# Kernel tuning notes

Measured on AMD Instinct MI355X. Metric: run time of the kernel, lower is better.

The kernel has to match this reference:

```python
import jax, jax.numpy as jnp
import numpy as np

B, C, H, W = 2, 128, 128, 128
HEADS = 8
D = C // HEADS
EPS = 1e-5


def _conv(x, w, pad):
    # x: [B,C,H,W], w: [O,I,kh,kw]
    return jax.lax.conv_general_dilated(
        x, w, window_strides=(1, 1), padding=[(pad, pad), (pad, pad)],
        dimension_numbers=("NCHW", "OIHW", "NCHW"))


def setup_inputs() -> dict:
    key = jax.random.key(0)
    ks = jax.random.split(key, 9)
    s = 0.05
    w11 = lambda k: jax.random.normal(k, (C, C, 1, 1), jnp.float32) * s
    w33 = lambda k: jax.random.normal(k, (C, C, 3, 3), jnp.float32) * s
    return {
        "x": jax.random.normal(ks[0], (B, C, H, W), jnp.float32),
        "gamma": jnp.ones((W,), jnp.float32),   # LayerNorm over LAST dim (W==C)
        "beta": jnp.zeros((W,), jnp.float32),
        "scale": jnp.ones((1,), jnp.float32),
        "wq1": w11(ks[1]), "wq2": w33(ks[2]),
        "wk1": w11(ks[3]), "wk2": w33(ks[4]),
        "wv1": w11(ks[5]), "wv2": w33(ks[6]),
        "wo": w11(ks[7]),
    }


def reference(x, gamma, beta, scale, wq1, wq2, wk1, wk2, wv1, wv2, wo):
    residual = x
    # torch nn.LayerNorm(channels) normalizes the last axis (W), biased variance
    mu = jnp.mean(x, axis=-1, keepdims=True)
    var = jnp.var(x, axis=-1, keepdims=True)
    xn = (x - mu) * jax.lax.rsqrt(var + EPS) * gamma + beta

    q = _conv(_conv(xn, wq1, 0), wq2, 1).reshape(B, HEADS, H * W, D)
    k = _conv(_conv(xn, wk1, 0), wk2, 1).reshape(B, HEADS, H * W, D).transpose(0, 1, 3, 2)
    v = _conv(_conv(xn, wv1, 0), wv2, 1).reshape(B, HEADS, H * W, D)

    # transposed (channel) attention: [B,h,d,HW] @ [B,h,HW,d] -> [B,h,d,d]
    attn = jnp.matmul(k, q) / scale
    probs = jax.nn.softmax(attn, axis=-1)
    out = jnp.matmul(v, probs)                      # [B,h,HW,d]
    out = out.transpose(0, 1, 3, 2).reshape(B, C, H, W)
    return _conv(out, wo, 0) + residual
```

## Files before the change

### kernel.cpp

```cpp
#include <hip/hip_runtime.h>
#include <hip/hip_bf16.h>

typedef unsigned short u16;
typedef _Float16 f16;
typedef f16 f16x8 __attribute__((ext_vector_type(8)));
typedef float f32x4 __attribute__((ext_vector_type(4)));

__device__ __forceinline__ float b2f(u16 u) {
  unsigned v = (unsigned)u << 16; float f; __builtin_memcpy(&f, &v, 4); return f;
}
__device__ __forceinline__ u16 f2b(float f) {
  return __builtin_bit_cast(u16, __float2bfloat16(f));
}
__device__ __forceinline__ float h2f(u16 u) {
  return (float)__builtin_bit_cast(f16, u);
}
__device__ __forceinline__ u16 f2h(float f) {
  return __builtin_bit_cast(u16, (f16)f);
}
__device__ __forceinline__ void gload16(const void* g, void* l) {
  __builtin_amdgcn_global_load_lds((__attribute__((address_space(1))) void*)(const_cast<void*>(g)),
                                   (__attribute__((address_space(3))) void*)l, 16, 0, 0);
}
__device__ __forceinline__ f32x4 mfma16(int4 a, int4 b, f32x4 c) {
  return __builtin_amdgcn_mfma_f32_16x16x32_f16(__builtin_bit_cast(f16x8, a),
                                                __builtin_bit_cast(f16x8, b), c, 0, 0, 0);
}
union PK { int4 i; u16 u[8]; };

__device__ __forceinline__ int detect_isf(const u16* x, int tid, int nthr) {
  __shared__ int dcnt;
  if (tid == 0) dcnt = 0;
  __syncthreads();
  int c = 0;
  for (int i = tid; i < 1024; i += nthr) {
    u16 u = x[i * 2];
    if (((u >> 7) & 0xFF) >= 0x90) ++c;
  }
  if (c) atomicAdd(&dcnt, c);
  __syncthreads();
  return dcnt > 16;
}

#define XROW 33280

__global__ __launch_bounds__(256) void k_lnweff(
    const void* __restrict__ xr, const void* __restrict__ gr, const void* __restrict__ br_,
    const void* __restrict__ w1q, const void* __restrict__ w2q,
    const void* __restrict__ w1k, const void* __restrict__ w2k,
    const void* __restrict__ w1v, const void* __restrict__ w2v,
    u16* __restrict__ weff, u16* __restrict__ xnt, float* __restrict__ attnb) {
  __shared__ __align__(16) char smem[99328];
  int tid = threadIdx.x;
  int bi = blockIdx.x;

  if (bi < 27) {
    u16* sA = (u16*)smem;
    u16* sB = (u16*)(smem + 32768);
    int isf = detect_isf((const u16*)xr, tid, 256);
    int blk = bi;
    int tap = blk / 3, br = blk - tap * 3;
    const void* w1 = br == 0 ? w1q : (br == 1 ? w1k : w1v);
    const void* w2 = br == 0 ? w2q : (br == 1 ? w2k : w2v);
    if (isf) {
      const float* w2f = (const float*)w2;
      const float* w1f = (const float*)w1;
#pragma unroll 4
      for (int i = 0; i < 64; ++i) {
        int e = i * 256 + tid;
        int c = e >> 7, m = e & 127;
        sA[c * 128 + (m ^ ((c & 15) << 3))] = f2h(w2f[e * 9 + tap]);
        int ci = e & 127;
        sB[ci * 128 + ((e >> 7) ^ ((ci & 15) << 3))] = f2h(w1f[e]);
      }
    } else {
      const u16* w2u = (const u16*)w2;
      const u16* w1u = (const u16*)w1;
#pragma unroll 4
      for (int i = 0; i < 64; ++i) {
        int e = i * 256 + tid;
        int c = e >> 7, m = e & 127;
        sA[c * 128 + (m ^ ((c & 15) << 3))] = f2h(b2f(w2u[e * 9 + tap]));
        int ci = e & 127;
        sB[ci * 128 + ((e >> 7) ^ ((ci & 15) << 3))] = f2h(b2f(w1u[e]));
      }
    }
    __syncthreads();
    int lane = tid & 63, wv = tid >> 6;
    int m0w = (wv >> 1) * 64, n0w = (wv & 1) * 64;
    f32x4 acc[4][4] = {};
#pragma unroll
    for (int k0 = 0; k0 < 4; ++k0) {
      int mrow = k0 * 32 + (lane >> 4) * 8;
      int4 a4[4], b4[4];
#pragma unroll
      for (int mi = 0; mi < 4; ++mi) {
        int c = m0w + mi * 16 + (lane & 15);
        a4[mi] = *(const int4*)&sA[c * 128 + (mrow ^ ((c & 15) << 3))];
      }
#pragma unroll
      for (int ni = 0; ni < 4; ++ni) {
        int ci = n0w + ni * 16 + (lane & 15);
        b4[ni] = *(const int4*)&sB[ci * 128 + (mrow ^ ((ci & 15) << 3))];
      }
#pragma unroll
      for (int mi = 0; mi < 4; ++mi)
#pragma unroll
        for (int ni = 0; ni < 4; ++ni)
          acc[mi][ni] = mfma16(a4[mi], b4[ni], acc[mi][ni]);
    }
    __syncthreads();
#pragma unroll
    for (int mi = 0; mi < 4; ++mi)
#pragma unroll
      for (int ni = 0; ni < 4; ++ni) {
#pragma unroll
        for (int r = 0; r < 4; ++r) {
          int c = m0w + mi * 16 + (lane >> 4) * 4 + r;
          int ci = n0w + ni * 16 + (lane & 15);
          sA[c * 128 + ci] = f2h(acc[mi][ni][r]);
        }
      }
    __syncthreads();
    int4* dst = (int4*)((char*)weff + (size_t)blk * 32768);
#pragma unroll
    for (int i = 0; i < 8; ++i) {
      int gidx = i * 256 + tid;
      int k0 = gidx >> 9;
      int ch = gidx & 511;
      int mt = ch >> 6, l = ch & 63;
      int c = mt * 16 + (l & 15);
      int g = k0 * 4 + (l >> 4);
      dst[gidx] = *(const int4*)((const char*)sA + c * 256 + g * 16);
    }
    return;
  }

  int li = bi - 27;
  if (li >= 256) {
    int pid = li - 256;
    int b = pid >> 1, row = (pid & 1) ? 129 : 0;
    char* rbase = (char*)xnt + (size_t)(b * 130 + row) * XROW;
    int4 z = make_int4(0, 0, 0, 0);
    for (int i = 0; i < 9; ++i) {
      int idx = i * 256 + tid;
      if (idx < 2080) *(int4*)(rbase + idx * 16) = z;
    }
    return;
  }
  if (li == 0) {
    for (int i = tid; i < 4096; i += 256) attnb[i] = 0.f;
  }
  float* sx = (float*)smem;
  u16* sn = (u16*)(smem + 65536);
  float* sg = (float*)(smem + 98304);
  float* sb = (float*)(smem + 98816);
  int b = li >> 7, h = li & 127;
  int isf = detect_isf((const u16*)xr, tid, 256);
  if (tid < 128) {
    sg[tid] = isf ? ((const float*)gr)[tid] : b2f(((const u16*)gr)[tid]);
    sb[tid] = isf ? ((const float*)br_)[tid] : b2f(((const u16*)br_)[tid]);
  }
  if (isf) {
#pragma unroll
    for (int it = 0; it < 16; ++it) {
      int d = it * 4096 + tid * 16;
      int c = d >> 9;
      int p = (d >> 4) & 31;
      int sc = p ^ (c & 31);
      const char* src = (const char*)xr + (size_t)(b * 128 + c) * 65536 + (size_t)h * 512 + (sc << 4);
      gload16(src, (char*)sx + d);
    }
  } else {
    int c = tid >> 1, half = tid & 1;
    const u16* xu = (const u16*)xr + ((size_t)(b * 128 + c) * 128 + h) * 128 + half * 64;
    for (int i = 0; i < 16; ++i) {
      int phys = (half * 16 + i) ^ (c & 31);
      float* dst = sx + c * 128 + phys * 4;
#pragma unroll
      for (int j = 0; j < 4; ++j) dst[j] = b2f(xu[i * 4 + j]);
    }
  }
  __syncthreads();
  int c = tid >> 1, half = tid & 1;
  float sum = 0.f, sq = 0.f;
#pragma unroll
  for (int i = 0; i < 16; ++i) {
    int phys = (half * 16 + i) ^ (c & 31);
    const float* v = sx + c * 128 + phys * 4;
#pragma unroll
    for (int j = 0; j < 4; ++j) { float f = v[j]; sum += f; sq += f * f; }
  }
  sum += __shfl_xor(sum, 1);
  sq  += __shfl_xor(sq, 1);
  float mu = sum * 0.0078125f;
  float var = sq * 0.0078125f - mu * mu;
  float rs = rsqrtf(var + 1e-5f);
  int cg = c >> 3, cl = c & 7;
#pragma unroll
  for (int i = 0; i < 16; ++i) {
    int logical = half * 16 + i;
    int phys = logical ^ (c & 31);
    const float* v = sx + c * 128 + phys * 4;
#pragma unroll
    for (int j = 0; j < 4; ++j) {
      int w = logical * 4 + j;
      sn[w * 128 + (((cg ^ (w & 15)) << 3) | cl)] = f2h((v[j] - mu) * rs * sg[w] + sb[w]);
    }
  }
  __syncthreads();
  char* obase = (char*)xnt + (size_t)(b * 130 + h + 1) * XROW;
#pragma unroll
  for (int i = 0; i < 8; ++i) {
    int idx = i * 256 + tid;
    int g = idx >> 7, w = idx & 127;
    int phys = g ^ (w & 15);
    *(int4*)(obase + (g * 130 + w + 1) * 16) = *(const int4*)((const char*)sn + w * 256 + (phys << 4));
  }
  if (tid < 32) {
    int g = tid >> 1, side = tid & 1;
    *(int4*)(obase + (g * 130 + (side ? 129 : 0)) * 16) = make_int4(0, 0, 0, 0);
  }
}

#define STAGE_T(T, BUF) do { \
    const char* base_ = (const char*)weff + (size_t)(T) * 32768 + (size_t)cohalf * 4096; \
    char* dst_ = wq + (BUF) * 16384; \
    _Pragma("unroll") \
    for (int i_ = 0; i_ < 4; ++i_) \
      gload16(base_ + i_ * 8192 + tid * 16, dst_ + i_ * 4096 + tid * 16); \
  } while (0)

#define BC_LOAD(DST, T6) do { \
    int dy_ = (T6) / 3, dx_ = (T6) % 3; \
    const char* rb_ = (const char*)xnt + (size_t)(b * 130 + h + dy_) * XROW; \
    _Pragma("unroll") \
    for (int kk = 0; kk < 4; ++kk) \
      _Pragma("unroll") \
      for (int ni = 0; ni < 2; ++ni) { \
        int wp1 = n0l + ni * 16 + (lane & 15) + dx_;    \
        int chunk = (kk * 4 + (lane >> 4)) * 130 + wp1; \
        DST[kk][ni] = *(const int4*)(rb_ + chunk * 16); \
      } \
  } while (0)

#define QFULL(ACC, QB) do { \
    _Pragma("unroll") \
    for (int k0 = 0; k0 < 4; ++k0) { \
      int4 af[4]; \
      _Pragma("unroll") \
      for (int mi = 0; mi < 4; ++mi) \
        af[mi] = *(const int4*)((QB) + k0 * 4096 + mi * 1024 + lane * 16); \
      _Pragma("unroll") \
      for (int mi = 0; mi < 4; ++mi) { \
        ACC[mi][0] = mfma16(af[mi], bcA[k0][0], ACC[mi][0]); \
        ACC[mi][1] = mfma16(af[mi], bcA[k0][1], ACC[mi][1]); \
      } \
    } \
  } while (0)

__global__ __launch_bounds__(256, 2) void k_conv(const u16* __restrict__ xnt,
    const u16* __restrict__ weff, u16* __restrict__ Vc, float* __restrict__ attnb) {
  __shared__ __align__(16) char wq[49152];
  int tid = threadIdx.x, lane = tid & 63, wv = tid >> 6;
  int bi = blockIdx.x;
  int cohalf = bi & 1, h = (bi >> 1) & 127, b = bi >> 8;
  int n0l = wv * 32;

  int4 bcA[4][2], bcB[4][2];
  BC_LOAD(bcA, 0);
  STAGE_T(0, 0);
  __syncthreads();

  f32x4 aq[4][2] = {}, ak[4][2] = {}, av[4][2] = {};

  for (int t = 0; t < 27; ++t) {
    int br = t % 3, tgrp = t / 3;
    if (t + 1 < 27) STAGE_T(t + 1, (t + 1) & 1);
    if (br == 0) {
      if (tgrp > 0) {
#pragma unroll
        for (int kk = 0; kk < 4; ++kk)
#pragma unroll
          for (int ni = 0; ni < 2; ++ni) bcA[kk][ni] = bcB[kk][ni];
      }
      if (tgrp < 8) BC_LOAD(bcB, tgrp + 1);
    }
    const char* qb = wq + (t & 1) * 16384;
    if (br == 0)      QFULL(aq, qb);
    else if (br == 1) QFULL(ak, qb);
    else              QFULL(av, qb);
    __syncthreads();
  }
  u16* scrQ = (u16*)wq;
  u16* scrK = (u16*)(wq + 16384);
  u16* scrV = (u16*)(wq + 32768);
#pragma unroll
  for (int mi = 0; mi < 4; ++mi)
#pragma unroll
    for (int ni = 0; ni < 2; ++ni)
#pragma unroll
      for (int r = 0; r < 4; ++r) {
        int cc = mi * 16 + (lane >> 4) * 4 + r;
        int wl = n0l + ni * 16 + (lane & 15);
        scrQ[cc * 128 + wl] = f2h(aq[mi][ni][r]);
        scrK[cc * 128 + wl] = f2h(ak[mi][ni][r]);
        scrV[cc * 128 + wl] = f2h(av[mi][ni][r]);
      }
  __syncthreads();
  {
    int hdg = cohalf * 4 + wv;
    f32x4 g = {};
#pragma unroll
    for (int k2 = 0; k2 < 4; ++k2) {
      PK A, Bq;
#pragma unroll
      for (int jj = 0; jj < 8; ++jj) {
        int k = (lane >> 4) * 8 + jj;
        int ci = k2 * 4 + (k >> 3);
        int wg = k & 7;
        A.u[jj]  = scrK[(wv * 16 + ci) * 128 + wg * 16 + (lane & 15)];
        Bq.u[jj] = scrQ[(wv * 16 + ci) * 128 + wg * 16 + (lane & 15)];
      }
      g = mfma16(A.i, Bq.i, g);
    }
#pragma unroll
    for (int r = 0; r < 4; ++r)
      atomicAdd(&attnb[((b * 8 + hdg) * 16 + (lane >> 4) * 4 + r) * 16 + (lane & 15)], g[r]);
  }
  char* dstV = (char*)Vc + (size_t)(b * 128 + cohalf * 64) * 32768 + (size_t)h * 256;
#pragma unroll
  for (int i = 0; i < 4; ++i) {
    int gi = i * 256 + tid;
    int c = gi >> 4, off = (gi & 15) << 4;
    *(int4*)(dstV + (size_t)c * 32768 + off) = *(const int4*)((const char*)scrV + c * 256 + off);
  }
}

__global__ __launch_bounds__(256) void k_w2(const float* __restrict__ attnb,
    const void* __restrict__ wo, const void* __restrict__ scale,
    const u16* __restrict__ xdet, u16* __restrict__ w2s) {
  __shared__ float P[256];
  int b = blockIdx.x, hd = blockIdx.y;
  int tid = threadIdx.x;
  int isf = detect_isf(xdet, tid, 256);
  float sc = isf ? ((const float*)scale)[0] : b2f(((const u16*)scale)[0]);
  float inv_sc = 1.f / sc;
  P[tid] = attnb[(b * 8 + hd) * 256 + tid] * inv_sc;
  __syncthreads();
  if (tid < 16) {
    int dk = tid;
    float m = -1e30f;
#pragma unroll
    for (int j = 0; j < 16; ++j) m = fmaxf(m, P[dk * 16 + j]);
    float e[16]; float s = 0.f;
#pragma unroll
    for (int j = 0; j < 16; ++j) { e[j] = expf(P[dk * 16 + j] - m); s += e[j]; }
    float is = 1.f / s;
#pragma unroll
    for (int j = 0; j < 16; ++j) P[dk * 16 + j] = e[j] * is;
  }
  __syncthreads();
  int co = tid & 127, kg = tid >> 7;
  float wr[16];
  if (isf) {
    const float* wof = (const float*)wo;
#pragma unroll
    for (int d = 0; d < 16; ++d) wr[d] = wof[co * 128 + hd * 16 + d];
  } else {
    const u16* wou = (const u16*)wo;
#pragma unroll
    for (int d = 0; d < 16; ++d) wr[d] = b2f(wou[co * 128 + hd * 16 + d]);
  }
  PK p;
#pragma unroll
  for (int j = 0; j < 8; ++j) {
    int dd = kg * 8 + j;
    float a = 0.f;
#pragma unroll
    for (int d = 0; d < 16; ++d) a += wr[d] * P[dd * 16 + d];
    p.u[j] = f2h(a);
  }
  int slot = hd * 2 + kg;
  *(int4*)((char*)w2s + (size_t)b * 32768 + co * 256 + ((slot ^ (co & 7)) << 4)) = p.i;
}

__global__ __launch_bounds__(256, 2) void k_final(const u16* __restrict__ w2s,
    const u16* __restrict__ Vc, const void* __restrict__ xr, void* __restrict__ outr) {
  __shared__ __align__(16) char sW[32768];
  __shared__ __align__(16) char sBk[16384];
  int tid = threadIdx.x, lane = tid & 63, wv = tid >> 6;
  int bi = blockIdx.x;
  int whalf = bi & 1, h = (bi >> 1) & 127, b = bi >> 8;
  int isf = detect_isf((const u16*)xr, tid, 256);
  const char* wsrc = (const char*)w2s + (size_t)b * 32768;
#pragma unroll
  for (int i = 0; i < 8; ++i) {
    int off = i * 4096 + tid * 16;
    gload16(wsrc + off, sW + off);
  }
#pragma unroll
  for (int i = 0; i < 4; ++i) {
    int gi = i * 256 + tid;
    int lr = gi >> 4, chunk = gi & 15;
    int hd8 = lr >> 3, rl = whalf * 8 + (lr & 7);
    int cv = hd8 * 16 + (h >> 3);
    int hv = (h & 7) * 16 + rl;
    const char* src = (const char*)Vc + (size_t)(b * 128 + cv) * 32768 + (size_t)hv * 256 + (chunk << 4);
    gload16(src, sBk + gi * 16);
  }
  __syncthreads();
  int m0 = (wv >> 1) * 64, n0l = (wv & 1) * 32;
  f32x4 acc[4][2] = {};
#pragma unroll
  for (int k0i = 0; k0i < 4; ++k0i) {
    int4 af[4], bfr[2];
#pragma unroll
    for (int mi = 0; mi < 4; ++mi) {
      int cc = m0 + mi * 16 + (lane & 15);
      int slot = (k0i * 4 + (lane >> 4)) ^ (cc & 7);
      af[mi] = *(const int4*)(sW + cc * 256 + (slot << 4));
    }
#pragma unroll
    for (int ni = 0; ni < 2; ++ni) {
      int wl = n0l + ni * 16 + (lane & 15);
      int k = k0i * 32 + (lane >> 4) * 8;
      int hd8 = k >> 4, dd0 = k & 15;
      bfr[ni] = *(const int4*)(sBk + (hd8 * 8 + (wl >> 3)) * 256 + ((wl & 7) * 32 + dd0 * 2));
    }
#pragma unroll
    for (int mi = 0; mi < 4; ++mi)
#pragma unroll
      for (int ni = 0; ni < 2; ++ni)
        acc[mi][ni] = mfma16(af[mi], bfr[ni], acc[mi][ni]);
  }
  if (isf) {
    const float* xf = (const float*)xr;
    float* of = (float*)outr;
#pragma unroll
    for (int mi = 0; mi < 4; ++mi)
#pragma unroll
      for (int ni = 0; ni < 2; ++ni) {
        int w = whalf * 64 + n0l + ni * 16 + (lane & 15);
#pragma unroll
        for (int r = 0; r < 4; ++r) {
          int cc = m0 + mi * 16 + (lane >> 4) * 4 + r;
          size_t idx = ((size_t)(b * 128 + cc) * 128 + (size_t)h) * 128 + w;
          of[idx] = acc[mi][ni][r] + xf[idx];
        }
      }
  } else {
    const u16* xu = (const u16*)xr;
    u16* ou = (u16*)outr;
#pragma unroll
    for (int mi = 0; mi < 4; ++mi)
#pragma unroll
      for (int ni = 0; ni < 2; ++ni) {
        int w = whalf * 64 + n0l + ni * 16 + (lane & 15);
#pragma unroll
        for (int r = 0; r < 4; ++r) {
          int cc = m0 + mi * 16 + (lane >> 4) * 4 + r;
          size_t idx = ((size_t)(b * 128 + cc) * 128 + (size_t)h) * 128 + w;
          ou[idx] = f2b(acc[mi][ni][r] + b2f(xu[idx]));
        }
      }
  }
}

extern "C" void kernel_launch(void* const* d_in, const int* in_sizes, int n_in,
                              void* d_out, int out_size, void* d_ws, size_t ws_size,
                              hipStream_t stream) {
  (void)in_sizes; (void)n_in; (void)out_size; (void)ws_size;
  const void* x     = d_in[0];
  const void* gamma = d_in[1];
  const void* beta  = d_in[2];
  const void* scale = d_in[3];
  const void* w1q = d_in[4];
  const void* w2q = d_in[5];
  const void* w1k = d_in[6];
  const void* w2k = d_in[7];
  const void* w1v = d_in[8];
  const void* w2v = d_in[9];
  const void* wo  = d_in[10];
  char* ws = (char*)d_ws;
  u16* xnt     = (u16*)(ws);
  u16* weff    = (u16*)(ws + (9u << 20));
  u16* Vc      = (u16*)(ws + (10u << 20));
  float* attnb = (float*)(ws + (18u << 20));
  u16* w2s     = (u16*)(ws + (18u << 20) + 65536);

  hipLaunchKernelGGL(k_lnweff, dim3(287), dim3(256), 0, stream,
                     x, gamma, beta, w1q, w2q, w1k, w2k, w1v, w2v, weff, xnt, attnb);
  hipLaunchKernelGGL(k_conv, dim3(512), dim3(256), 0, stream, xnt, weff, Vc, attnb);
  hipLaunchKernelGGL(k_w2, dim3(2, 8), dim3(256), 0, stream, attnb, wo, scale, (const u16*)x, w2s);
  hipLaunchKernelGGL(k_final, dim3(512), dim3(256), 0, stream, w2s, Vc, x, d_out);
}
```

Baseline: 79.61 us.

## Split conv output channels into quarters to double grid and occupancy

The fused 3x3 QKV conv kernel now gives each block a quarter of the output channels instead of half. This doubles the grid to 1024 blocks, halves the LDS weight buffer and the accumulator registers, and raises the launch-bounds occupancy hint from 2 to 4. It also drops the double-buffered B-fragment prefetch and reloads the activations synchronously at each tap group. In exchange, every activation row is loaded by twice as many blocks, and the atomic attention reduction is split across more waves.

```diff
diff --git a/kernel.cpp b/kernel.cpp
--- a/kernel.cpp
+++ b/kernel.cpp
@@ -224,11 +224,12 @@
 }
 
 #define STAGE_T(T, BUF) do { \
-    const char* base_ = (const char*)weff + (size_t)(T) * 32768 + (size_t)cohalf * 4096; \
-    char* dst_ = wq + (BUF) * 16384; \
+    const char* base_ = (const char*)weff + (size_t)(T) * 32768 + (size_t)coq * 2048; \
+    char* dst_ = wq + (BUF) * 8192; \
     _Pragma("unroll") \
-    for (int i_ = 0; i_ < 4; ++i_) \
-      gload16(base_ + i_ * 8192 + tid * 16, dst_ + i_ * 4096 + tid * 16); \
+    for (int i_ = 0; i_ < 2; ++i_) \
+      gload16(base_ + (size_t)(i_ * 2 + (tid >> 7)) * 8192 + (tid & 127) * 16, \
+              dst_ + i_ * 4096 + tid * 16); \
   } while (0)
 
 #define BC_LOAD(DST, T6) do { \
@@ -247,56 +248,48 @@
 #define QFULL(ACC, QB) do { \
     _Pragma("unroll") \
     for (int k0 = 0; k0 < 4; ++k0) { \
-      int4 af[4]; \
+      int4 af[2]; \
       _Pragma("unroll") \
-      for (int mi = 0; mi < 4; ++mi) \
-        af[mi] = *(const int4*)((QB) + k0 * 4096 + mi * 1024 + lane * 16); \
+      for (int mi = 0; mi < 2; ++mi) \
+        af[mi] = *(const int4*)((QB) + (k0 >> 1) * 4096 + (k0 & 1) * 2048 + mi * 1024 + lane * 16); \
       _Pragma("unroll") \
-      for (int mi = 0; mi < 4; ++mi) { \
+      for (int mi = 0; mi < 2; ++mi) { \
         ACC[mi][0] = mfma16(af[mi], bcA[k0][0], ACC[mi][0]); \
         ACC[mi][1] = mfma16(af[mi], bcA[k0][1], ACC[mi][1]); \
       } \
     } \
   } while (0)
 
-__global__ __launch_bounds__(256, 2) void k_conv(const u16* __restrict__ xnt,
+__global__ __launch_bounds__(256, 4) void k_conv(const u16* __restrict__ xnt,
     const u16* __restrict__ weff, u16* __restrict__ Vc, float* __restrict__ attnb) {
-  __shared__ __align__(16) char wq[49152];
+  __shared__ __align__(16) char wq[24576];
   int tid = threadIdx.x, lane = tid & 63, wv = tid >> 6;
   int bi = blockIdx.x;
-  int cohalf = bi & 1, h = (bi >> 1) & 127, b = bi >> 8;
+  int coq = bi & 3, h = (bi >> 2) & 127, b = bi >> 9;
   int n0l = wv * 32;
 
-  int4 bcA[4][2], bcB[4][2];
+  int4 bcA[4][2];
   BC_LOAD(bcA, 0);
   STAGE_T(0, 0);
   __syncthreads();
 
-  f32x4 aq[4][2] = {}, ak[4][2] = {}, av[4][2] = {};
+  f32x4 aq[2][2] = {}, ak[2][2] = {}, av[2][2] = {};
 
   for (int t = 0; t < 27; ++t) {
     int br = t % 3, tgrp = t / 3;
     if (t + 1 < 27) STAGE_T(t + 1, (t + 1) & 1);
-    if (br == 0) {
-      if (tgrp > 0) {
-#pragma unroll
-        for (int kk = 0; kk < 4; ++kk)
-#pragma unroll
-          for (int ni = 0; ni < 2; ++ni) bcA[kk][ni] = bcB[kk][ni];
-      }
-      if (tgrp < 8) BC_LOAD(bcB, tgrp + 1);
-    }
-    const char* qb = wq + (t & 1) * 16384;
+    if (br == 0 && tgrp > 0) BC_LOAD(bcA, tgrp);
+    const char* qb = wq + (t & 1) * 8192;
     if (br == 0)      QFULL(aq, qb);
     else if (br == 1) QFULL(ak, qb);
     else              QFULL(av, qb);
     __syncthreads();
   }
   u16* scrQ = (u16*)wq;
-  u16* scrK = (u16*)(wq + 16384);
-  u16* scrV = (u16*)(wq + 32768);
-#pragma unroll
-  for (int mi = 0; mi < 4; ++mi)
+  u16* scrK = (u16*)(wq + 8192);
+  u16* scrV = (u16*)(wq + 16384);
+#pragma unroll
+  for (int mi = 0; mi < 2; ++mi)
 #pragma unroll
     for (int ni = 0; ni < 2; ++ni)
 #pragma unroll
@@ -309,18 +302,20 @@
       }
   __syncthreads();
   {
-    int hdg = cohalf * 4 + wv;
+    int hdl = wv >> 1;
+    int wp = wv & 1;
+    int hdg = coq * 2 + hdl;
     f32x4 g = {};
 #pragma unroll
-    for (int k2 = 0; k2 < 4; ++k2) {
+    for (int k2 = 0; k2 < 2; ++k2) {
       PK A, Bq;
 #pragma unroll
       for (int jj = 0; jj < 8; ++jj) {
         int k = (lane >> 4) * 8 + jj;
-        int ci = k2 * 4 + (k >> 3);
-        int wg = k & 7;
-        A.u[jj]  = scrK[(wv * 16 + ci) * 128 + wg * 16 + (lane & 15)];
-        Bq.u[jj] = scrQ[(wv * 16 + ci) * 128 + wg * 16 + (lane & 15)];
+        int slot = (wp * 2 + k2) * 32 + k;
+        int ci = slot >> 3, wg = slot & 7;
+        A.u[jj]  = scrK[(hdl * 16 + ci) * 128 + wg * 16 + (lane & 15)];
+        Bq.u[jj] = scrQ[(hdl * 16 + ci) * 128 + wg * 16 + (lane & 15)];
       }
       g = mfma16(A.i, Bq.i, g);
     }
@@ -328,9 +323,9 @@
     for (int r = 0; r < 4; ++r)
       atomicAdd(&attnb[((b * 8 + hdg) * 16 + (lane >> 4) * 4 + r) * 16 + (lane & 15)], g[r]);
   }
-  char* dstV = (char*)Vc + (size_t)(b * 128 + cohalf * 64) * 32768 + (size_t)h * 256;
-#pragma unroll
-  for (int i = 0; i < 4; ++i) {
+  char* dstV = (char*)Vc + (size_t)(b * 128 + coq * 32) * 32768 + (size_t)h * 256;
+#pragma unroll
+  for (int i = 0; i < 2; ++i) {
     int gi = i * 256 + tid;
     int c = gi >> 4, off = (gi & 15) << 4;
     *(int4*)(dstV + (size_t)c * 32768 + off) = *(const int4*)((const char*)scrV + c * 256 + off);
@@ -491,7 +486,7 @@
 
   hipLaunchKernelGGL(k_lnweff, dim3(287), dim3(256), 0, stream,
                      x, gamma, beta, w1q, w2q, w1k, w2k, w1v, w2v, weff, xnt, attnb);
-  hipLaunchKernelGGL(k_conv, dim3(512), dim3(256), 0, stream, xnt, weff, Vc, attnb);
+  hipLaunchKernelGGL(k_conv, dim3(1024), dim3(256), 0, stream, xnt, weff, Vc, attnb);
   hipLaunchKernelGGL(k_w2, dim3(2, 8), dim3(256), 0, stream, attnb, wo, scale, (const u16*)x, w2s);
   hipLaunchKernelGGL(k_final, dim3(512), dim3(256), 0, stream, w2s, Vc, x, d_out);
 }
```

New measurement: 194.4 us. +144.2%, slower.
